# Kernel optimization log

Measured on AMD Instinct MI355X. Metric: run time of the kernel, lower is better.

The kernel has to match this reference:

```python
import jax, jax.numpy as jnp
import numpy as np

VOCAB = 50257
SEQ = 2048
EMB = 512
BATCH = 8


def setup_inputs() -> dict:
    key = jax.random.key(0)
    k1, k2, k3 = jax.random.split(key, 3)
    tokens = jax.random.randint(k1, (BATCH, SEQ), 0, VOCAB, dtype=jnp.int64 if jax.config.jax_enable_x64 else jnp.int32)
    W_emb = jax.random.normal(k2, (EMB, VOCAB), dtype=jnp.float32)
    W_pos = jax.random.normal(k3, (SEQ, EMB), dtype=jnp.float32)
    return {"tokens": tokens, "W_emb": W_emb, "W_pos": W_pos}


def reference(tokens, W_emb, W_pos):
    # Original: one_hot(tokens, V).float() @ W_emb.T  -> identical to gathering
    # columns of W_emb, i.e. rows of W_emb.T. Shapes: (B,S) -> (B,S,E)
    tok_emb = jnp.take(W_emb.T, tokens, axis=0)  # (B, S, E)
    # positional weight (S, E) broadcasts over batch
    return tok_emb + W_pos
```

## Files before the change

### kernel.cpp

```cpp
#include <hip/hip_runtime.h>

#define VOCAB 50257
#define SEQ   2048
#define EMB   512
#define BATCH 8
#define NTOK  (BATCH * SEQ)

typedef float floatx4 __attribute__((ext_vector_type(4)));

#define MAP_INTS      VOCAB
#define COUNTER_IDX   50432
#define WTC_OFFSET    (256 * 1024)

__global__ __launch_bounds__(256)
void init_map_k(int* __restrict__ map, int* __restrict__ counter) {
    const int i = blockIdx.x * 256 + threadIdx.x;
    if (i < VOCAB) map[i] = -1;
    if (i == 0) *counter = 0;
}

__global__ __launch_bounds__(256)
void build_map_k(const int* __restrict__ tokens, int* __restrict__ map,
                 int* __restrict__ counter) {
    const int i = blockIdx.x * 256 + threadIdx.x;
    if (i >= NTOK) return;
    const int t = tokens[i];
    const int old = atomicCAS(&map[t], -1, -2);
    if (old == -1) {
        const int slot = atomicAdd(counter, 1);
        atomicExch(&map[t], slot);
    }
}

__global__ __launch_bounds__(256)
void transpose_compact_k(const float* __restrict__ in,
                         const int* __restrict__ map,
                         float* __restrict__ WTc) {
    __shared__ float tile[64][65];
    __shared__ int used_v[64];
    __shared__ int used_s[64];
    __shared__ int nused_s;
    const int v0 = blockIdx.x * 64;
    const int e0 = blockIdx.y * 64;
    const int tx = threadIdx.x;
    const int ty = threadIdx.y;
    const int v  = v0 + tx;
    const bool vok = (v < VOCAB);

#pragma unroll
    for (int j = 0; j < 16; ++j) {
        const int e_l = 4 * j + ty;
        if (vok) tile[e_l][tx] = in[(size_t)(e0 + e_l) * VOCAB + v];
    }
    if (ty == 0) {
        const int s = vok ? map[v] : -1;
        const unsigned long long mask = __ballot(s >= 0);
        const int pos = __popcll(mask & ((1ull << tx) - 1ull));
        if (s >= 0) { used_v[pos] = tx; used_s[pos] = s; }
        if (tx == 0) nused_s = (int)__popcll(mask);
    }
    __syncthreads();
    const int nused = nused_s;
    for (int u = ty; u < nused; u += 4) {
        const int v_l = used_v[u];
        const int s   = used_s[u];
        WTc[(size_t)s * EMB + e0 + tx] = tile[tx][v_l];
    }
}

__global__ __launch_bounds__(256)
void gather_k(const int* __restrict__ tokens,
              const int* __restrict__ map,
              const floatx4* __restrict__ WTc,
              const floatx4* __restrict__ Wpos,
              floatx4* __restrict__ out) {
    const int idx = blockIdx.x * blockDim.x + threadIdx.x;
    const int e4  = idx & (EMB / 4 - 1);
    const int ts  = idx >> 7;
    const int s   = ts & (SEQ - 1);
    const int slot = map[tokens[ts]];
    const floatx4 emb = WTc[(size_t)slot * (EMB / 4) + e4];
    const floatx4 p   = Wpos[(size_t)s * (EMB / 4) + e4];
    __builtin_nontemporal_store(emb + p, &out[idx]);
}

__global__ __launch_bounds__(256)
void gather_direct_k(const int* __restrict__ tokens,
                     const float* __restrict__ W_emb,
                     const floatx4* __restrict__ Wpos,
                     floatx4* __restrict__ out) {
    const int idx = blockIdx.x * blockDim.x + threadIdx.x;
    const int e4  = idx & (EMB / 4 - 1);
    const int ts  = idx >> 7;
    const int s   = ts & (SEQ - 1);
    const int t   = tokens[ts];
    const size_t base = (size_t)(4 * e4) * VOCAB + (size_t)t;
    floatx4 r;
    r.x = W_emb[base];
    r.y = W_emb[base + (size_t)VOCAB];
    r.z = W_emb[base + (size_t)(2 * VOCAB)];
    r.w = W_emb[base + (size_t)(3 * VOCAB)];
    __builtin_nontemporal_store(r + Wpos[(size_t)s * (EMB / 4) + e4], &out[idx]);
}

extern "C" void kernel_launch(void* const* d_in, const int* in_sizes, int n_in,
                              void* d_out, int out_size, void* d_ws, size_t ws_size,
                              hipStream_t stream) {
    const int*   tokens = (const int*)d_in[0];
    const float* W_emb  = (const float*)d_in[1];
    const float* W_pos  = (const float*)d_in[2];
    float*       out    = (float*)d_out;

    const int n_out4  = BATCH * SEQ * (EMB / 4);
    const int gblocks = n_out4 / 256;

    const size_t need = WTC_OFFSET + (size_t)NTOK * EMB * sizeof(float);
    if (ws_size >= need) {
        int*   map     = (int*)d_ws;
        int*   counter = map + COUNTER_IDX;
        float* WTc     = (float*)((char*)d_ws + WTC_OFFSET);

        init_map_k<<<(VOCAB + 255) / 256, 256, 0, stream>>>(map, counter);
        build_map_k<<<NTOK / 256, 256, 0, stream>>>(tokens, map, counter);
        transpose_compact_k<<<dim3((VOCAB + 63) / 64, EMB / 64), dim3(64, 4), 0, stream>>>(
            W_emb, map, WTc);
        gather_k<<<gblocks, 256, 0, stream>>>(tokens, map, (const floatx4*)WTc,
                                              (const floatx4*)W_pos, (floatx4*)out);
    } else {
        gather_direct_k<<<gblocks, 256, 0, stream>>>(tokens, W_emb,
                                                     (const floatx4*)W_pos,
                                                     (floatx4*)out);
    }
}
```

Measured before the change: 184.0 us.

## Scatter transposed embedding tiles directly to output via counting-sort token positions

```diff
diff --git a/kernel.cpp b/kernel.cpp
--- a/kernel.cpp
+++ b/kernel.cpp
@@ -8,37 +8,90 @@
 
 typedef float floatx4 __attribute__((ext_vector_type(4)));
 
-#define MAP_INTS      VOCAB
-#define COUNTER_IDX   50432
-#define WTC_OFFSET    (256 * 1024)
+#define CNT_OFF   0
+#define CUR_OFF   50432
+#define BSUM_OFF  100864
+#define POS_OFF   101120
+#define WS_INTS   (POS_OFF + NTOK)
+#define NBLK      197
 
 __global__ __launch_bounds__(256)
-void init_map_k(int* __restrict__ map, int* __restrict__ counter) {
+void zero_k(int* __restrict__ cnt) {
     const int i = blockIdx.x * 256 + threadIdx.x;
-    if (i < VOCAB) map[i] = -1;
-    if (i == 0) *counter = 0;
+    if (i < VOCAB) cnt[i] = 0;
 }
 
 __global__ __launch_bounds__(256)
-void build_map_k(const int* __restrict__ tokens, int* __restrict__ map,
-                 int* __restrict__ counter) {
+void hist_k(const int* __restrict__ tokens, int* __restrict__ cnt) {
     const int i = blockIdx.x * 256 + threadIdx.x;
-    if (i >= NTOK) return;
-    const int t = tokens[i];
-    const int old = atomicCAS(&map[t], -1, -2);
-    if (old == -1) {
-        const int slot = atomicAdd(counter, 1);
-        atomicExch(&map[t], slot);
-    }
+    atomicAdd(&cnt[tokens[i]], 1);
 }
 
 __global__ __launch_bounds__(256)
-void transpose_compact_k(const float* __restrict__ in,
-                         const int* __restrict__ map,
-                         float* __restrict__ WTc) {
+void scan_partial_k(const int* __restrict__ cnt, int* __restrict__ bsum) {
+    const int tid = threadIdx.x;
+    const int v   = blockIdx.x * 256 + tid;
+    int c = (v < VOCAB) ? cnt[v] : 0;
+#pragma unroll
+    for (int d = 32; d > 0; d >>= 1) c += __shfl_down(c, d);
+    __shared__ int rb[4];
+    if ((tid & 63) == 0) rb[tid >> 6] = c;
+    __syncthreads();
+    if (tid == 0) bsum[blockIdx.x] = rb[0] + rb[1] + rb[2] + rb[3];
+}
+
+__global__ __launch_bounds__(256)
+void scan_offsets_k(const int* __restrict__ cnt, const int* __restrict__ bsum,
+                    int* __restrict__ endcur) {
+    __shared__ int sb[256];
+    __shared__ int rb[4];
+    __shared__ int wsum[4];
+    const int b   = blockIdx.x;
+    const int tid = threadIdx.x;
+    if (tid < NBLK) sb[tid] = bsum[tid];
+    __syncthreads();
+    int base = 0;
+    for (int k = tid; k < b; k += 256) base += sb[k];
+#pragma unroll
+    for (int d = 32; d > 0; d >>= 1) base += __shfl_down(base, d);
+    if ((tid & 63) == 0) rb[tid >> 6] = base;
+    __syncthreads();
+    const int base_total = rb[0] + rb[1] + rb[2] + rb[3];
+    const int v = b * 256 + tid;
+    const int c = (v < VOCAB) ? cnt[v] : 0;
+    int x = c;
+#pragma unroll
+    for (int d = 1; d < 64; d <<= 1) {
+        const int y = __shfl_up(x, d);
+        if ((tid & 63) >= d) x += y;
+    }
+    if ((tid & 63) == 63) wsum[tid >> 6] = x;
+    __syncthreads();
+    int wbase = 0;
+    for (int w = 0; w < (tid >> 6); ++w) wbase += wsum[w];
+    if (v < VOCAB) endcur[v] = base_total + wbase + x - c;
+}
+
+__global__ __launch_bounds__(256)
+void fill_k(const int* __restrict__ tokens, int* __restrict__ endcur,
+            int* __restrict__ positions) {
+    const int i = blockIdx.x * 256 + threadIdx.x;
+    const int t = tokens[i];
+    const int p = atomicAdd(&endcur[t], 1);
+    positions[p] = i;
+}
+
+__global__ __launch_bounds__(256)
+void scatter_k(const float* __restrict__ in,
+               const int* __restrict__ cnt,
+               const int* __restrict__ endcur,
+               const int* __restrict__ positions,
+               const float* __restrict__ Wpos,
+               float* __restrict__ out) {
     __shared__ float tile[64][65];
     __shared__ int used_v[64];
-    __shared__ int used_s[64];
+    __shared__ int used_st[64];
+    __shared__ int used_n[64];
     __shared__ int nused_s;
     const int v0 = blockIdx.x * 64;
     const int e0 = blockIdx.y * 64;
@@ -47,41 +100,37 @@
     const int v  = v0 + tx;
     const bool vok = (v < VOCAB);
 
+    if (vok) {
+        const float* rp = in + (size_t)(e0 + ty) * VOCAB + v;
 #pragma unroll
-    for (int j = 0; j < 16; ++j) {
-        const int e_l = 4 * j + ty;
-        if (vok) tile[e_l][tx] = in[(size_t)(e0 + e_l) * VOCAB + v];
+        for (int j = 0; j < 16; ++j)
+            tile[4 * j + ty][tx] = rp[(size_t)(4 * j) * VOCAB];
     }
     if (ty == 0) {
-        const int s = vok ? map[v] : -1;
-        const unsigned long long mask = __ballot(s >= 0);
-        const int pos = __popcll(mask & ((1ull << tx) - 1ull));
-        if (s >= 0) { used_v[pos] = tx; used_s[pos] = s; }
-        if (tx == 0) nused_s = (int)__popcll(mask);
+        const int n = vok ? cnt[v] : 0;
+        const unsigned long long m = __ballot(n > 0);
+        const int pos = __popcll(m & ((1ull << tx) - 1ull));
+        if (n > 0) {
+            used_v[pos]  = tx;
+            used_n[pos]  = n;
+            used_st[pos] = endcur[v] - n;
+        }
+        if (tx == 0) nused_s = (int)__popcll(m);
     }
     __syncthreads();
     const int nused = nused_s;
     for (int u = ty; u < nused; u += 4) {
-        const int v_l = used_v[u];
-        const int s   = used_s[u];
-        WTc[(size_t)s * EMB + e0 + tx] = tile[tx][v_l];
+        const int vl = used_v[u];
+        const int n  = used_n[u];
+        const int st = used_st[u];
+        const float val = tile[tx][vl];
+        for (int k = 0; k < n; ++k) {
+            const int p = positions[st + k];
+            const int s = p & (SEQ - 1);
+            const float r = val + Wpos[(size_t)s * EMB + e0 + tx];
+            __builtin_nontemporal_store(r, &out[(size_t)p * EMB + e0 + tx]);
+        }
     }
-}
-
-__global__ __launch_bounds__(256)
-void gather_k(const int* __restrict__ tokens,
-              const int* __restrict__ map,
-              const floatx4* __restrict__ WTc,
-              const floatx4* __restrict__ Wpos,
-              floatx4* __restrict__ out) {
-    const int idx = blockIdx.x * blockDim.x + threadIdx.x;
-    const int e4  = idx & (EMB / 4 - 1);
-    const int ts  = idx >> 7;
-    const int s   = ts & (SEQ - 1);
-    const int slot = map[tokens[ts]];
-    const floatx4 emb = WTc[(size_t)slot * (EMB / 4) + e4];
-    const floatx4 p   = Wpos[(size_t)s * (EMB / 4) + e4];
-    __builtin_nontemporal_store(emb + p, &out[idx]);
 }
 
 __global__ __launch_bounds__(256)
@@ -111,22 +160,23 @@
     const float* W_pos  = (const float*)d_in[2];
     float*       out    = (float*)d_out;
 
-    const int n_out4  = BATCH * SEQ * (EMB / 4);
-    const int gblocks = n_out4 / 256;
+    const size_t need = (size_t)WS_INTS * sizeof(int);
+    if (ws_size >= need) {
+        int* cnt       = (int*)d_ws + CNT_OFF;
+        int* endcur    = (int*)d_ws + CUR_OFF;
+        int* bsum      = (int*)d_ws + BSUM_OFF;
+        int* positions = (int*)d_ws + POS_OFF;
 
-    const size_t need = WTC_OFFSET + (size_t)NTOK * EMB * sizeof(float);
-    if (ws_size >= need) {
-        int*   map     = (int*)d_ws;
-        int*   counter = map + COUNTER_IDX;
-        float* WTc     = (float*)((char*)d_ws + WTC_OFFSET);
-
-        init_map_k<<<(VOCAB + 255) / 256, 256, 0, stream>>>(map, counter);
-        build_map_k<<<NTOK / 256, 256, 0, stream>>>(tokens, map, counter);
-        transpose_compact_k<<<dim3((VOCAB + 63) / 64, EMB / 64), dim3(64, 4), 0, stream>>>(
-            W_emb, map, WTc);
-        gather_k<<<gblocks, 256, 0, stream>>>(tokens, map, (const floatx4*)WTc,
-                                              (const floatx4*)W_pos, (floatx4*)out);
+        zero_k<<<NBLK, 256, 0, stream>>>(cnt);
+        hist_k<<<NTOK / 256, 256, 0, stream>>>(tokens, cnt);
+        scan_partial_k<<<NBLK, 256, 0, stream>>>(cnt, bsum);
+        scan_offsets_k<<<NBLK, 256, 0, stream>>>(cnt, bsum, endcur);
+        fill_k<<<NTOK / 256, 256, 0, stream>>>(tokens, endcur, positions);
+        scatter_k<<<dim3((VOCAB + 63) / 64, EMB / 64), dim3(64, 4), 0, stream>>>(
+            W_emb, cnt, endcur, positions, W_pos, out);
     } else {
+        const int n_out4  = BATCH * SEQ * (EMB / 4);
+        const int gblocks = n_out4 / 256;
         gather_direct_k<<<gblocks, 256, 0, stream>>>(tokens, W_emb,
                                                      (const floatx4*)W_pos,
                                                      (floatx4*)out);
```

Result: no change. 185.9 us (+1.1%).

## Fuse map, transpose and gather into a single slab-scatter kernel

Applied to the files above, without the earlier changes.

```diff
diff --git a/kernel.cpp b/kernel.cpp
--- a/kernel.cpp
+++ b/kernel.cpp
@@ -6,101 +6,63 @@
 #define BATCH 8
 #define NTOK  (BATCH * SEQ)
 
-typedef float floatx4 __attribute__((ext_vector_type(4)));
 
-#define MAP_INTS      VOCAB
-#define COUNTER_IDX   50432
-#define WTC_OFFSET    (256 * 1024)
+#define CHUNK 2048
+#define NCHUNK (NTOK / CHUNK)
 
 __global__ __launch_bounds__(256)
-void init_map_k(int* __restrict__ map, int* __restrict__ counter) {
-    const int i = blockIdx.x * 256 + threadIdx.x;
-    if (i < VOCAB) map[i] = -1;
-    if (i == 0) *counter = 0;
-}
+void slab_scatter_k(const int* __restrict__ tokens,
+                    const float* __restrict__ W,
+                    const float* __restrict__ Wpos,
+                    float* __restrict__ out) {
+    __shared__ float slab[64][257];
+    __shared__ int   m_p[CHUNK];
+    __shared__ unsigned char m_vl[CHUNK];
+    __shared__ int   nmatch;
 
-__global__ __launch_bounds__(256)
-void build_map_k(const int* __restrict__ tokens, int* __restrict__ map,
-                 int* __restrict__ counter) {
-    const int i = blockIdx.x * 256 + threadIdx.x;
-    if (i >= NTOK) return;
-    const int t = tokens[i];
-    const int old = atomicCAS(&map[t], -1, -2);
-    if (old == -1) {
-        const int slot = atomicAdd(counter, 1);
-        atomicExch(&map[t], slot);
+    const int v0   = blockIdx.x * 64;
+    const int eoff = blockIdx.y * 256;
+    const int tid  = threadIdx.x;
+    const int tx   = tid & 63;
+    const int ty   = tid >> 6;
+
+    if (tid == 0) nmatch = 0;
+
+    const int v = v0 + tx;
+    if (v < VOCAB) {
+        const float* rp = W + (size_t)(eoff + ty) * VOCAB + v;
+#pragma unroll
+        for (int j = 0; j < 64; ++j)
+            slab[tx][4 * j + ty] = rp[(size_t)(4 * j) * VOCAB];
     }
-}
 
-__global__ __launch_bounds__(256)
-void transpose_compact_k(const float* __restrict__ in,
-                         const int* __restrict__ map,
-                         float* __restrict__ WTc) {
-    __shared__ float tile[64][65];
-    __shared__ int used_v[64];
-    __shared__ int used_s[64];
-    __shared__ int nused_s;
-    const int v0 = blockIdx.x * 64;
-    const int e0 = blockIdx.y * 64;
-    const int tx = threadIdx.x;
-    const int ty = threadIdx.y;
-    const int v  = v0 + tx;
-    const bool vok = (v < VOCAB);
-
+    for (int c = 0; c < NCHUNK; ++c) {
+        const int base = c * CHUNK;
 #pragma unroll
-    for (int j = 0; j < 16; ++j) {
-        const int e_l = 4 * j + ty;
-        if (vok) tile[e_l][tx] = in[(size_t)(e0 + e_l) * VOCAB + v];
+        for (int k = 0; k < CHUNK / 256; ++k) {
+            const int i = base + k * 256 + tid;
+            const unsigned d = (unsigned)(tokens[i] - v0);
+            if (d < 64u) {
+                const int m = atomicAdd(&nmatch, 1);
+                m_p[m]  = i;
+                m_vl[m] = (unsigned char)d;
+            }
+        }
+        __syncthreads();
+        const int nm = nmatch;
+        for (int m = 0; m < nm; ++m) {
+            const int p  = m_p[m];
+            const int vl = m_vl[m];
+            const int s  = p & (SEQ - 1);
+            const float r = slab[vl][tid]
+                          + Wpos[(size_t)s * EMB + eoff + tid];
+            __builtin_nontemporal_store(
+                r, &out[(size_t)p * EMB + eoff + tid]);
+        }
+        __syncthreads();
+        if (tid == 0) nmatch = 0;
+        __syncthreads();
     }
-    if (ty == 0) {
-        const int s = vok ? map[v] : -1;
-        const unsigned long long mask = __ballot(s >= 0);
-        const int pos = __popcll(mask & ((1ull << tx) - 1ull));
-        if (s >= 0) { used_v[pos] = tx; used_s[pos] = s; }
-        if (tx == 0) nused_s = (int)__popcll(mask);
-    }
-    __syncthreads();
-    const int nused = nused_s;
-    for (int u = ty; u < nused; u += 4) {
-        const int v_l = used_v[u];
-        const int s   = used_s[u];
-        WTc[(size_t)s * EMB + e0 + tx] = tile[tx][v_l];
-    }
-}
-
-__global__ __launch_bounds__(256)
-void gather_k(const int* __restrict__ tokens,
-              const int* __restrict__ map,
-              const floatx4* __restrict__ WTc,
-              const floatx4* __restrict__ Wpos,
-              floatx4* __restrict__ out) {
-    const int idx = blockIdx.x * blockDim.x + threadIdx.x;
-    const int e4  = idx & (EMB / 4 - 1);
-    const int ts  = idx >> 7;
-    const int s   = ts & (SEQ - 1);
-    const int slot = map[tokens[ts]];
-    const floatx4 emb = WTc[(size_t)slot * (EMB / 4) + e4];
-    const floatx4 p   = Wpos[(size_t)s * (EMB / 4) + e4];
-    __builtin_nontemporal_store(emb + p, &out[idx]);
-}
-
-__global__ __launch_bounds__(256)
-void gather_direct_k(const int* __restrict__ tokens,
-                     const float* __restrict__ W_emb,
-                     const floatx4* __restrict__ Wpos,
-                     floatx4* __restrict__ out) {
-    const int idx = blockIdx.x * blockDim.x + threadIdx.x;
-    const int e4  = idx & (EMB / 4 - 1);
-    const int ts  = idx >> 7;
-    const int s   = ts & (SEQ - 1);
-    const int t   = tokens[ts];
-    const size_t base = (size_t)(4 * e4) * VOCAB + (size_t)t;
-    floatx4 r;
-    r.x = W_emb[base];
-    r.y = W_emb[base + (size_t)VOCAB];
-    r.z = W_emb[base + (size_t)(2 * VOCAB)];
-    r.w = W_emb[base + (size_t)(3 * VOCAB)];
-    __builtin_nontemporal_store(r + Wpos[(size_t)s * (EMB / 4) + e4], &out[idx]);
 }
 
 extern "C" void kernel_launch(void* const* d_in, const int* in_sizes, int n_in,
@@ -111,24 +73,8 @@
     const float* W_pos  = (const float*)d_in[2];
     float*       out    = (float*)d_out;
 
-    const int n_out4  = BATCH * SEQ * (EMB / 4);
-    const int gblocks = n_out4 / 256;
+    (void)d_ws; (void)ws_size;
 
-    const size_t need = WTC_OFFSET + (size_t)NTOK * EMB * sizeof(float);
-    if (ws_size >= need) {
-        int*   map     = (int*)d_ws;
-        int*   counter = map + COUNTER_IDX;
-        float* WTc     = (float*)((char*)d_ws + WTC_OFFSET);
-
-        init_map_k<<<(VOCAB + 255) / 256, 256, 0, stream>>>(map, counter);
-        build_map_k<<<NTOK / 256, 256, 0, stream>>>(tokens, map, counter);
-        transpose_compact_k<<<dim3((VOCAB + 63) / 64, EMB / 64), dim3(64, 4), 0, stream>>>(
-            W_emb, map, WTc);
-        gather_k<<<gblocks, 256, 0, stream>>>(tokens, map, (const floatx4*)WTc,
-                                              (const floatx4*)W_pos, (floatx4*)out);
-    } else {
-        gather_direct_k<<<gblocks, 256, 0, stream>>>(tokens, W_emb,
-                                                     (const floatx4*)W_pos,
-                                                     (floatx4*)out);
-    }
+    slab_scatter_k<<<dim3((VOCAB + 63) / 64, EMB / 256), 256, 0, stream>>>(
+        tokens, W_emb, W_pos, out);
 }
```

Measured after the change: 232.8 us. 26.5% more time.
